# Optimization experiments

Hardware: AMD Instinct MI355X
Metric: run time of the kernel (lower is better)

## Reference

```python
import jax, jax.numpy as jnp
import numpy as np

N = 50000   # num nodes
E = 800000  # num edges
D_IN, D_HID, D_OUT = 128, 128, 64


def setup_inputs() -> dict:
    key = jax.random.key(0)
    ks = jax.random.split(key, 10)
    x = jax.random.normal(ks[0], (N, D_IN), dtype=jnp.float32)
    edge_index = jax.random.randint(ks[1], (2, E), 0, N, dtype=jnp.int32)
    edge_weight = jax.random.uniform(ks[2], (E,), dtype=jnp.float32)
    def lin(k, fan_in, fan_out):
        bound = 1.0 / np.sqrt(fan_in)
        kw, kb = jax.random.split(k)
        W = jax.random.uniform(kw, (fan_out, fan_in), minval=-bound, maxval=bound, dtype=jnp.float32)
        b = jax.random.uniform(kb, (fan_out,), minval=-bound, maxval=bound, dtype=jnp.float32)
        return W, b
    W0, b0 = lin(ks[3], 2 * D_IN, D_HID)
    W1, b1 = lin(ks[4], 2 * D_HID, D_HID)
    W2, b2 = lin(ks[5], 2 * D_HID, D_OUT)
    return {"x": x, "edge_index": edge_index, "edge_weight": edge_weight,
            "W0": W0, "b0": b0, "W1": W1, "b1": b1, "W2": W2, "b2": b2}


def _sage_layer(x, row, col, ew, W, b):
    # weighted mean aggregation over incoming edges (dst = row, src = col)
    n = x.shape[0]
    msg = x[col] * ew[:, None]                      # [E, D] gather + scale
    agg = jax.ops.segment_sum(msg, row, num_segments=n)    # [N, D]
    deg = jax.ops.segment_sum(ew, row, num_segments=n)     # [N]
    deg = jnp.clip(deg, 1.0, None)[:, None]
    h = jnp.concatenate([x, agg / deg], axis=-1)    # [N, 2D]
    return h @ W.T + b


def reference(x, edge_index, edge_weight, W0, b0, W1, b1, W2, b2):
    row, col = edge_index[0], edge_index[1]
    h = jax.nn.relu(_sage_layer(x, row, col, edge_weight, W0, b0))
    h = jax.nn.relu(_sage_layer(h, row, col, edge_weight, W1, b1))
    return _sage_layer(h, row, col, edge_weight, W2, b2)
```

## Files before the change

### kernel.cpp

```cpp
#include <hip/hip_runtime.h>


#define D 128
#define K2 256
#define NQ 4
#define QW 12500
#define NBUCK 196
#define SCAP 5120
#define CH 2048

typedef __attribute__((ext_vector_type(8))) short short8;
typedef __attribute__((ext_vector_type(4))) float floatx4;

__device__ inline unsigned short rne_bf16(float f) {
    unsigned int u = __float_as_uint(f);
    u += 0x7fffu + ((u >> 16) & 1u);
    return (unsigned short)(u >> 16);
}

__device__ inline int quarter_of(int c) {
    return (c >= 2 * QW) ? ((c >= 3 * QW) ? 3 : 2) : ((c >= QW) ? 1 : 0);
}

__global__ void prep_kernel(const float* __restrict__ x, unsigned short* __restrict__ x_hi,
                            const float* __restrict__ W0, const float* __restrict__ W1,
                            const float* __restrict__ W2,
                            unsigned short* __restrict__ h0, unsigned short* __restrict__ l0,
                            unsigned short* __restrict__ h1, unsigned short* __restrict__ l1,
                            unsigned short* __restrict__ h2, unsigned short* __restrict__ l2,
                            const int* __restrict__ row, const int* __restrict__ col,
                            int* __restrict__ cnt, int n4, int E) {
    int b = blockIdx.x;
    int tid = threadIdx.x;
    if (b < 6250) {
        int i = b * 256 + tid;
        if (i < n4) {
            float4 v = reinterpret_cast<const float4*>(x)[i];
            ushort4 o;
            o.x = rne_bf16(v.x); o.y = rne_bf16(v.y); o.z = rne_bf16(v.z); o.w = rne_bf16(v.w);
            reinterpret_cast<ushort4*>(x_hi)[i] = o;
        }
    } else if (b < 6570) {
        int i = (b - 6250) * 256 + tid;
        const float* w; unsigned short *hi, *lo; int sidx, didx;
        if (i < 32768)      { w = W0; hi = h0; lo = l0; sidx = i; didx = i; }
        else if (i < 65536) { w = W1; hi = h1; lo = l1; sidx = i - 32768; didx = sidx; }
        else if (i < 81920) {
            w = W2; hi = h2; lo = l2;
            int i2 = i - 65536;
            int r = i2 >> 7, k = i2 & 127;
            sidx = (r < 64) ? (r * 256 + k) : ((r - 64) * 256 + 128 + k);
            didx = i2;
        }
        else return;
        float f = w[sidx];
        unsigned short h = rne_bf16(f);
        float fh = __uint_as_float(((unsigned int)h) << 16);
        hi[didx] = h;
        lo[didx] = rne_bf16(f - fh);
    } else {
        int e = (b - 6570) * 256 + tid;
        if (e < E) {
            int key = row[e] * NQ + quarter_of(col[e]);
            atomicAdd(&cnt[key], 1);
        }
    }
}

__global__ void scan1_kernel(const int* __restrict__ cnt, int* __restrict__ rowptr,
                             int* __restrict__ bsum, int NB) {
    __shared__ int s[256];
    int tid = threadIdx.x;
    int gid = blockIdx.x * 256 + tid;
    int v = (gid < NB) ? cnt[gid] : 0;
    s[tid] = v;
    __syncthreads();
    for (int off = 1; off < 256; off <<= 1) {
        int t = (tid >= off) ? s[tid - off] : 0;
        __syncthreads();
        s[tid] += t;
        __syncthreads();
    }
    if (gid < NB) rowptr[gid] = s[tid] - v;
    if (tid == 255) bsum[blockIdx.x] = s[255];
}

__global__ void scan2_kernel(int* __restrict__ bsum, int* __restrict__ boff, int nb) {
    __shared__ int s[1024];
    int tid = threadIdx.x;
    int v = (tid < nb) ? bsum[tid] : 0;
    s[tid] = v;
    __syncthreads();
    for (int off = 1; off < 1024; off <<= 1) {
        int t = (tid >= off) ? s[tid - off] : 0;
        __syncthreads();
        s[tid] += t;
        __syncthreads();
    }
    if (tid < nb) boff[tid] = s[tid] - v;
}

__global__ void scan3_kernel(int* __restrict__ rowptr, const int* __restrict__ boff,
                             int* __restrict__ cursor, int NB, int E) {
    int gid = blockIdx.x * 256 + threadIdx.x;
    if (gid < NB) {
        int v = rowptr[gid] + boff[gid >> 8];
        rowptr[gid] = v;
        cursor[gid] = v;
    } else if (gid == NB) {
        rowptr[NB] = E;
    }
}

__global__ __launch_bounds__(512) void scatter_bin(
    const int* __restrict__ row, const int* __restrict__ col,
    const float* __restrict__ ew, int* __restrict__ scnt,
    int* __restrict__ cursor, int2* __restrict__ stage,
    int2* __restrict__ ep, int E) {
    __shared__ int cnt[NBUCK];
    __shared__ int base[NBUCK];
    __shared__ int gb[NBUCK];
    __shared__ int scn[256];
    __shared__ int2 sdata[CH];
    __shared__ unsigned char sbkt[CH];
    int tid = threadIdx.x;
    for (int i = tid; i < NBUCK; i += 512) cnt[i] = 0;
    __syncthreads();

    int e0 = blockIdx.x * CH + tid * 4;
    int rw4[4], c4[4], w4[4], b4[4], lo4[4];
    bool act = (e0 < E);
    if (act) {
        int4 r = *reinterpret_cast<const int4*>(row + e0);
        int4 c = *reinterpret_cast<const int4*>(col + e0);
        float4 w = *reinterpret_cast<const float4*>(ew + e0);
        rw4[0] = r.x; rw4[1] = r.y; rw4[2] = r.z; rw4[3] = r.w;
        c4[0] = c.x; c4[1] = c.y; c4[2] = c.z; c4[3] = c.w;
        w4[0] = __float_as_int(w.x); w4[1] = __float_as_int(w.y);
        w4[2] = __float_as_int(w.z); w4[3] = __float_as_int(w.w);
#pragma unroll
        for (int u = 0; u < 4; u++) {
            b4[u] = rw4[u] >> 8;
            lo4[u] = atomicAdd(&cnt[b4[u]], 1);
        }
    }
    __syncthreads();

    if (tid < 256) scn[tid] = (tid < NBUCK) ? cnt[tid] : 0;
    __syncthreads();
    for (int off = 1; off < 256; off <<= 1) {
        int t = (tid >= off && tid < 256) ? scn[tid - off] : 0;
        __syncthreads();
        if (tid < 256) scn[tid] += t;
        __syncthreads();
    }
    if (tid < NBUCK) {
        base[tid] = scn[tid] - cnt[tid];
        gb[tid] = (cnt[tid] > 0) ? atomicAdd(&scnt[tid], cnt[tid]) : 0;
    }
    __syncthreads();

    if (act) {
#pragma unroll
        for (int u = 0; u < 4; u++) {
            int slot = base[b4[u]] + lo4[u];
            int key = ((rw4[u] & 255) << 2) | quarter_of(c4[u]);
            sdata[slot] = make_int2((key << 16) | c4[u], w4[u]);
            sbkt[slot] = (unsigned char)b4[u];
        }
    }
    __syncthreads();

    int total = scn[255];
    for (int i = tid; i < total; i += 512) {
        int b = sbkt[i];
        int2 rec = sdata[i];
        int pos = gb[b] + (i - base[b]);
        if (pos < SCAP) {
            stage[b * SCAP + pos] = rec;
        } else {
            int binidx = (b << 10) + ((unsigned int)rec.x >> 16);
            int p = atomicAdd(&cursor[binidx], 1);
            ep[p] = make_int2(rec.x & 0xFFFF, rec.y);
        }
    }
}

__global__ __launch_bounds__(512) void scatter_drain(
    const int2* __restrict__ stage, const int* __restrict__ scnt,
    const int* __restrict__ cursor, int2* __restrict__ ep, int NBtot) {
    __shared__ int cur[1024];
    int b = blockIdx.x;
    int tid = threadIdx.x;
    for (int i = tid; i < 1024; i += 512) {
        int g = (b << 10) + i;
        cur[i] = (g < NBtot) ? cursor[g] : 0;
    }
    __syncthreads();
    int m = scnt[b];
    if (m > SCAP) m = SCAP;
    for (int i = tid; i < m; i += 512) {
        int2 rec = stage[b * SCAP + i];
        int key = (unsigned int)rec.x >> 16;
        int p = atomicAdd(&cur[key], 1);
        ep[p] = make_int2(rec.x & 0xFFFF, rec.y);
    }
}

__device__ inline void accum8(float* acc, uint4 a, float w) {
    acc[0] += __uint_as_float(a.x << 16) * w;
    acc[1] += __uint_as_float(a.x & 0xffff0000u) * w;
    acc[2] += __uint_as_float(a.y << 16) * w;
    acc[3] += __uint_as_float(a.y & 0xffff0000u) * w;
    acc[4] += __uint_as_float(a.z << 16) * w;
    acc[5] += __uint_as_float(a.z & 0xffff0000u) * w;
    acc[6] += __uint_as_float(a.w << 16) * w;
    acc[7] += __uint_as_float(a.w & 0xffff0000u) * w;
}

__global__ void gather_agg_bf(const unsigned short* __restrict__ src, const int* __restrict__ rowptr4,
                              const int2* __restrict__ ep, unsigned short* __restrict__ agg, int N) {
    long long t = (long long)blockIdx.x * blockDim.x + threadIdx.x;
    int wid = (int)(t >> 6);
    int lane = threadIdx.x & 63;
    int slot = lane >> 4;
    int fl = lane & 15;
    int n = wid * 4 + slot;
    if (n >= N) return;
    int beg = rowptr4[n * 4], end = rowptr4[n * 4 + 4];
    float acc[8];
#pragma unroll
    for (int j = 0; j < 8; j++) acc[j] = 0.f;
    float ds = 0.f;
    int e = beg;
    for (; e + 7 < end; e += 8) {
        int2 p[8];
#pragma unroll
        for (int u = 0; u < 8; u++) p[u] = ep[e + u];
        uint4 a[8];
#pragma unroll
        for (int u = 0; u < 8; u++)
            a[u] = *reinterpret_cast<const uint4*>(src + (size_t)p[u].x * D + fl * 8);
#pragma unroll
        for (int u = 0; u < 8; u++) {
            float w = __int_as_float(p[u].y);
            accum8(acc, a[u], w);
            ds += w;
        }
    }
    for (; e + 3 < end; e += 4) {
        int2 p[4];
#pragma unroll
        for (int u = 0; u < 4; u++) p[u] = ep[e + u];
#pragma unroll
        for (int u = 0; u < 4; u++) {
            uint4 a = *reinterpret_cast<const uint4*>(src + (size_t)p[u].x * D + fl * 8);
            float w = __int_as_float(p[u].y);
            accum8(acc, a, w);
            ds += w;
        }
    }
    for (; e < end; ++e) {
        int2 p = ep[e];
        uint4 a = *reinterpret_cast<const uint4*>(src + (size_t)p.x * D + fl * 8);
        float w = __int_as_float(p.y);
        accum8(acc, a, w);
        ds += w;
    }
    float inv = 1.0f / (ds > 1.f ? ds : 1.f);
    uint4 o;
    o.x = (unsigned int)rne_bf16(acc[0] * inv) | ((unsigned int)rne_bf16(acc[1] * inv) << 16);
    o.y = (unsigned int)rne_bf16(acc[2] * inv) | ((unsigned int)rne_bf16(acc[3] * inv) << 16);
    o.z = (unsigned int)rne_bf16(acc[4] * inv) | ((unsigned int)rne_bf16(acc[5] * inv) << 16);
    o.w = (unsigned int)rne_bf16(acc[6] * inv) | ((unsigned int)rne_bf16(acc[7] * inv) << 16);
    *reinterpret_cast<uint4*>(agg + (size_t)n * D + fl * 8) = o;
}

template<bool RELU, bool BF16OUT, int OSTRIDE>
__global__ __launch_bounds__(256) void sage_gemm(
    const unsigned short* __restrict__ src, const unsigned short* __restrict__ agg,
    const unsigned short* __restrict__ Whi, const unsigned short* __restrict__ Wlo,
    const float* __restrict__ bias, float* __restrict__ outf,
    unsigned short* __restrict__ outb, int N) {
    __shared__ short sW[2][32][260];
    int tid = threadIdx.x;
    int c0 = blockIdx.y * 32;

    for (int i = tid; i < 2048; i += 256) {
        int h = i >> 10;
        int rem = i & 1023;
        int r = rem & 31;
        int k8 = rem >> 5;
        const unsigned short* wp = (h ? Wlo : Whi) + (size_t)(c0 + r) * K2 + k8 * 8;
        *reinterpret_cast<uint4*>(&sW[h][r][k8 * 8]) = *reinterpret_cast<const uint4*>(wp);
    }
    __syncthreads();

    int lane = tid & 63;
    int wv = tid >> 6;
    int nlane = lane & 15;
    int quad = lane >> 4;
    int m0 = blockIdx.x * 128 + wv * 32;
    int r0 = m0 + nlane;      if (r0 >= N) r0 = N - 1;
    int r1 = m0 + 16 + nlane; if (r1 >= N) r1 = N - 1;

    short8 a[2][8];
#pragma unroll
    for (int ks = 0; ks < 8; ks++) {
        int k0 = ks * 32;
        const unsigned short* p0 = (k0 < D) ? (src + (size_t)r0 * D + k0)
                                            : (agg + (size_t)r0 * D + (k0 - D));
        const unsigned short* p1 = (k0 < D) ? (src + (size_t)r1 * D + k0)
                                            : (agg + (size_t)r1 * D + (k0 - D));
        a[0][ks] = *reinterpret_cast<const short8*>(p0 + quad * 8);
        a[1][ks] = *reinterpret_cast<const short8*>(p1 + quad * 8);
    }

    floatx4 acc[2][2];
#pragma unroll
    for (int mt = 0; mt < 2; mt++)
#pragma unroll
        for (int nt = 0; nt < 2; nt++) acc[mt][nt] = (floatx4){0.f, 0.f, 0.f, 0.f};

#pragma unroll
    for (int ks = 0; ks < 8; ks++) {
        int k0 = ks * 32;
#pragma unroll
        for (int nt = 0; nt < 2; nt++) {
            short8 bh = *reinterpret_cast<const short8*>(&sW[0][nt * 16 + nlane][k0 + quad * 8]);
            short8 bl = *reinterpret_cast<const short8*>(&sW[1][nt * 16 + nlane][k0 + quad * 8]);
            acc[0][nt] = __builtin_amdgcn_mfma_f32_16x16x32_bf16(a[0][ks], bh, acc[0][nt], 0, 0, 0);
            acc[0][nt] = __builtin_amdgcn_mfma_f32_16x16x32_bf16(a[0][ks], bl, acc[0][nt], 0, 0, 0);
            acc[1][nt] = __builtin_amdgcn_mfma_f32_16x16x32_bf16(a[1][ks], bh, acc[1][nt], 0, 0, 0);
            acc[1][nt] = __builtin_amdgcn_mfma_f32_16x16x32_bf16(a[1][ks], bl, acc[1][nt], 0, 0, 0);
        }
    }

#pragma unroll
    for (int nt = 0; nt < 2; nt++) {
        int c = c0 + nt * 16 + nlane;
        float bb = bias[c];
#pragma unroll
        for (int mt = 0; mt < 2; mt++) {
#pragma unroll
            for (int r = 0; r < 4; r++) {
                int node = m0 + mt * 16 + quad * 4 + r;
                if (node < N) {
                    float y = acc[mt][nt][r] + bb;
                    if (RELU) y = y > 0.f ? y : 0.f;
                    if (BF16OUT) outb[(size_t)node * OSTRIDE + c] = rne_bf16(y);
                    else         outf[(size_t)node * OSTRIDE + c] = y;
                }
            }
        }
    }
}

__global__ __launch_bounds__(256) void sage_gemm2(
    const unsigned short* __restrict__ h1, const unsigned short* __restrict__ Whi,
    const unsigned short* __restrict__ Wlo, const float* __restrict__ b2,
    float* __restrict__ ytop2, unsigned short* __restrict__ z2, int N) {
    __shared__ short sW[2][32][132];
    int tid = threadIdx.x;
    int c0 = blockIdx.y * 32;

    for (int i = tid; i < 1024; i += 256) {
        int h = i >> 9;
        int rem = i & 511;
        int r = rem & 31;
        int k8 = rem >> 5;
        const unsigned short* wp = (h ? Wlo : Whi) + (size_t)(c0 + r) * 128 + k8 * 8;
        *reinterpret_cast<uint4*>(&sW[h][r][k8 * 8]) = *reinterpret_cast<const uint4*>(wp);
    }
    __syncthreads();

    int lane = tid & 63;
    int wv = tid >> 6;
    int nlane = lane & 15;
    int quad = lane >> 4;
    int m0 = blockIdx.x * 128 + wv * 32;
    int r0 = m0 + nlane;      if (r0 >= N) r0 = N - 1;
    int r1 = m0 + 16 + nlane; if (r1 >= N) r1 = N - 1;

    short8 a[2][4];
#pragma unroll
    for (int ks = 0; ks < 4; ks++) {
        a[0][ks] = *reinterpret_cast<const short8*>(h1 + (size_t)r0 * D + ks * 32 + quad * 8);
        a[1][ks] = *reinterpret_cast<const short8*>(h1 + (size_t)r1 * D + ks * 32 + quad * 8);
    }

    floatx4 acc[2][2];
#pragma unroll
    for (int mt = 0; mt < 2; mt++)
#pragma unroll
        for (int nt = 0; nt < 2; nt++) acc[mt][nt] = (floatx4){0.f, 0.f, 0.f, 0.f};

#pragma unroll
    for (int ks = 0; ks < 4; ks++) {
        int k0 = ks * 32;
#pragma unroll
        for (int nt = 0; nt < 2; nt++) {
            short8 bh = *reinterpret_cast<const short8*>(&sW[0][nt * 16 + nlane][k0 + quad * 8]);
            short8 bl = *reinterpret_cast<const short8*>(&sW[1][nt * 16 + nlane][k0 + quad * 8]);
            acc[0][nt] = __builtin_amdgcn_mfma_f32_16x16x32_bf16(a[0][ks], bh, acc[0][nt], 0, 0, 0);
            acc[0][nt] = __builtin_amdgcn_mfma_f32_16x16x32_bf16(a[0][ks], bl, acc[0][nt], 0, 0, 0);
            acc[1][nt] = __builtin_amdgcn_mfma_f32_16x16x32_bf16(a[1][ks], bh, acc[1][nt], 0, 0, 0);
            acc[1][nt] = __builtin_amdgcn_mfma_f32_16x16x32_bf16(a[1][ks], bl, acc[1][nt], 0, 0, 0);
        }
    }

#pragma unroll
    for (int nt = 0; nt < 2; nt++) {
        int c = c0 + nt * 16 + nlane;
#pragma unroll
        for (int mt = 0; mt < 2; mt++) {
#pragma unroll
            for (int r = 0; r < 4; r++) {
                int node = m0 + mt * 16 + quad * 4 + r;
                if (node < N) {
                    float v = acc[mt][nt][r];
                    if (c < 64) ytop2[(size_t)node * 64 + c] = v + b2[c];
                    else        z2[(size_t)node * 64 + (c - 64)] = rne_bf16(v);
                }
            }
        }
    }
}

__global__ void gather_out(const unsigned short* __restrict__ z2, const int* __restrict__ rowptr4,
                           const int2* __restrict__ ep, const float* __restrict__ ytop2,
                           float* __restrict__ out, int N) {
    long long t = (long long)blockIdx.x * blockDim.x + threadIdx.x;
    int wid = (int)(t >> 6);
    int lane = threadIdx.x & 63;
    int slot = lane >> 3;
    int fl = lane & 7;
    int n = wid * 8 + slot;
    if (n >= N) return;
    int beg = rowptr4[n * 4], end = rowptr4[n * 4 + 4];
    float acc[8];
#pragma unroll
    for (int j = 0; j < 8; j++) acc[j] = 0.f;
    float ds = 0.f;
    int e = beg;
    for (; e + 7 < end; e += 8) {
        int2 p[8];
#pragma unroll
        for (int u = 0; u < 8; u++) p[u] = ep[e + u];
        uint4 a[8];
#pragma unroll
        for (int u = 0; u < 8; u++)
            a[u] = *reinterpret_cast<const uint4*>(z2 + (size_t)p[u].x * 64 + fl * 8);
#pragma unroll
        for (int u = 0; u < 8; u++) {
            float w = __int_as_float(p[u].y);
            accum8(acc, a[u], w);
            ds += w;
        }
    }
    for (; e < end; ++e) {
        int2 p = ep[e];
        uint4 a = *reinterpret_cast<const uint4*>(z2 + (size_t)p.x * 64 + fl * 8);
        float w = __int_as_float(p.y);
        accum8(acc, a, w);
        ds += w;
    }
    float inv = 1.0f / (ds > 1.f ? ds : 1.f);
    const float* yt = ytop2 + (size_t)n * 64 + fl * 8;
    float* op = out + (size_t)n * 64 + fl * 8;
    float4 t0 = *reinterpret_cast<const float4*>(yt);
    float4 t1 = *reinterpret_cast<const float4*>(yt + 4);
    float4 o0 = make_float4(t0.x + acc[0] * inv, t0.y + acc[1] * inv,
                            t0.z + acc[2] * inv, t0.w + acc[3] * inv);
    float4 o1 = make_float4(t1.x + acc[4] * inv, t1.y + acc[5] * inv,
                            t1.z + acc[6] * inv, t1.w + acc[7] * inv);
    *reinterpret_cast<float4*>(op) = o0;
    *reinterpret_cast<float4*>(op + 4) = o1;
}

extern "C" void kernel_launch(void* const* d_in, const int* in_sizes, int n_in,
                              void* d_out, int out_size, void* d_ws, size_t ws_size,
                              hipStream_t stream) {
    const float* x  = (const float*)d_in[0];
    const int*   ei = (const int*)d_in[1];
    const float* ew = (const float*)d_in[2];
    const float* W0 = (const float*)d_in[3];
    const float* b0 = (const float*)d_in[4];
    const float* W1 = (const float*)d_in[5];
    const float* b1 = (const float*)d_in[6];
    const float* W2 = (const float*)d_in[7];
    const float* b2 = (const float*)d_in[8];
    float* out = (float*)d_out;

    const int N = 50000;
    const int E = in_sizes[2];
    const int NB = N * NQ;
    const int* row = ei;
    const int* col = ei + E;

    char* base = (char*)d_ws;
    size_t ND = (size_t)N * D;
    unsigned short* x_hi   = (unsigned short*)base;               base += ND * 2;
    unsigned short* h0_hi  = (unsigned short*)base;               base += ND * 2;
    unsigned short* h1_hi  = (unsigned short*)base;               base += ND * 2;
    unsigned short* agg_hi = (unsigned short*)base;               base += ND * 2;
    int2* ep               = (int2*)base;                         base += (size_t)E * 8;
    int* rowptr4           = (int*)base;                          base += (size_t)(NB + 1) * 4;
    unsigned short* W0hi   = (unsigned short*)base;               base += 128 * 256 * 2;
    unsigned short* W0lo   = (unsigned short*)base;               base += 128 * 256 * 2;
    unsigned short* W1hi   = (unsigned short*)base;               base += 128 * 256 * 2;
    unsigned short* W1lo   = (unsigned short*)base;               base += 128 * 256 * 2;
    unsigned short* W2Chi  = (unsigned short*)base;               base += 128 * 128 * 2;
    unsigned short* W2Clo  = (unsigned short*)base;               base += 128 * 128 * 2;

    int* cnt    = (int*)h0_hi;
    int* cursor = cnt + NB;
    int* bsum   = cursor + NB;
    int* boff   = bsum + 1024;
    int* scnt   = boff + 1024;

    int2* stage = (int2*)h1_hi;

    float* ytop2          = (float*)agg_hi;
    unsigned short* z2    = (unsigned short*)h0_hi;

    int nbScan = (NB + 255) / 256;

    hipMemsetAsync(cnt, 0, (size_t)(2 * NB + 2304) * sizeof(int), stream);
    int n4 = (int)(ND / 4);
    prep_kernel<<<9695, 256, 0, stream>>>(x, x_hi, W0, W1, W2,
        W0hi, W0lo, W1hi, W1lo, W2Chi, W2Clo, row, col, cnt, n4, E);

    scan1_kernel<<<nbScan, 256, 0, stream>>>(cnt, rowptr4, bsum, NB);
    scan2_kernel<<<1, 1024, 0, stream>>>(bsum, boff, nbScan);
    scan3_kernel<<<(NB + 256) / 256 + 1, 256, 0, stream>>>(rowptr4, boff, cursor, NB, E);
    scatter_bin<<<(E + CH - 1) / CH, 512, 0, stream>>>(row, col, ew, scnt, cursor, stage, ep, E);
    scatter_drain<<<NBUCK, 512, 0, stream>>>(stage, scnt, cursor, ep, NB);

    int nWaves = (N + 3) / 4;
    int aggBlocks = (int)(((long long)nWaves * 64 + 255) / 256);
    int nodeTiles = (N + 127) / 128;
    dim3 g128(nodeTiles, 4);

    gather_agg_bf<<<aggBlocks, 256, 0, stream>>>(x_hi, rowptr4, ep, agg_hi, N);
    sage_gemm<true, true, D><<<g128, 256, 0, stream>>>(
        x_hi, agg_hi, W0hi, W0lo, b0, nullptr, h0_hi, N);

    gather_agg_bf<<<aggBlocks, 256, 0, stream>>>(h0_hi, rowptr4, ep, agg_hi, N);
    sage_gemm<true, true, D><<<g128, 256, 0, stream>>>(
        h0_hi, agg_hi, W1hi, W1lo, b1, nullptr, h1_hi, N);

    sage_gemm2<<<g128, 256, 0, stream>>>(h1_hi, W2Chi, W2Clo, b2, ytop2, z2, N);
    int nWaves2 = (N + 7) / 8;
    int outBlocks = (int)(((long long)nWaves2 * 64 + 255) / 256);
    gather_out<<<outBlocks, 256, 0, stream>>>(z2, rowptr4, ep, ytop2, out, N);
}
```

Baseline: 307.2 us.

## Fuse neighbor aggregation and SAGE GEMM into one per-tile layer kernel

Replaces the separate gather-aggregate kernel and the GEMM kernel for layers 0 and 1 with one kernel per 128-node tile. Each tile aggregates neighbor rows into shared memory and then runs the MFMA GEMM over all four 32-column output tiles, reloading weights each pass. This removes the global round trip of the aggregate buffer and two launches per layer. In exchange the grid is much smaller (about 391 blocks of 512 threads), weights are streamed serially per block, and gather latency can no longer overlap with GEMM work from other launches.

```diff
diff --git a/kernel.cpp b/kernel.cpp
--- a/kernel.cpp
+++ b/kernel.cpp
@@ -218,141 +218,135 @@
     acc[7] += __uint_as_float(a.w & 0xffff0000u) * w;
 }
 
-__global__ void gather_agg_bf(const unsigned short* __restrict__ src, const int* __restrict__ rowptr4,
-                              const int2* __restrict__ ep, unsigned short* __restrict__ agg, int N) {
-    long long t = (long long)blockIdx.x * blockDim.x + threadIdx.x;
-    int wid = (int)(t >> 6);
-    int lane = threadIdx.x & 63;
-    int slot = lane >> 4;
-    int fl = lane & 15;
-    int n = wid * 4 + slot;
-    if (n >= N) return;
-    int beg = rowptr4[n * 4], end = rowptr4[n * 4 + 4];
-    float acc[8];
-#pragma unroll
-    for (int j = 0; j < 8; j++) acc[j] = 0.f;
-    float ds = 0.f;
-    int e = beg;
-    for (; e + 7 < end; e += 8) {
-        int2 p[8];
-#pragma unroll
-        for (int u = 0; u < 8; u++) p[u] = ep[e + u];
-        uint4 a[8];
-#pragma unroll
-        for (int u = 0; u < 8; u++)
-            a[u] = *reinterpret_cast<const uint4*>(src + (size_t)p[u].x * D + fl * 8);
-#pragma unroll
-        for (int u = 0; u < 8; u++) {
-            float w = __int_as_float(p[u].y);
-            accum8(acc, a[u], w);
-            ds += w;
-        }
-    }
-    for (; e + 3 < end; e += 4) {
-        int2 p[4];
-#pragma unroll
-        for (int u = 0; u < 4; u++) p[u] = ep[e + u];
-#pragma unroll
-        for (int u = 0; u < 4; u++) {
-            uint4 a = *reinterpret_cast<const uint4*>(src + (size_t)p[u].x * D + fl * 8);
-            float w = __int_as_float(p[u].y);
-            accum8(acc, a, w);
-            ds += w;
-        }
-    }
-    for (; e < end; ++e) {
-        int2 p = ep[e];
-        uint4 a = *reinterpret_cast<const uint4*>(src + (size_t)p.x * D + fl * 8);
-        float w = __int_as_float(p.y);
-        accum8(acc, a, w);
-        ds += w;
-    }
-    float inv = 1.0f / (ds > 1.f ? ds : 1.f);
-    uint4 o;
-    o.x = (unsigned int)rne_bf16(acc[0] * inv) | ((unsigned int)rne_bf16(acc[1] * inv) << 16);
-    o.y = (unsigned int)rne_bf16(acc[2] * inv) | ((unsigned int)rne_bf16(acc[3] * inv) << 16);
-    o.z = (unsigned int)rne_bf16(acc[4] * inv) | ((unsigned int)rne_bf16(acc[5] * inv) << 16);
-    o.w = (unsigned int)rne_bf16(acc[6] * inv) | ((unsigned int)rne_bf16(acc[7] * inv) << 16);
-    *reinterpret_cast<uint4*>(agg + (size_t)n * D + fl * 8) = o;
-}
-
-template<bool RELU, bool BF16OUT, int OSTRIDE>
-__global__ __launch_bounds__(256) void sage_gemm(
-    const unsigned short* __restrict__ src, const unsigned short* __restrict__ agg,
-    const unsigned short* __restrict__ Whi, const unsigned short* __restrict__ Wlo,
-    const float* __restrict__ bias, float* __restrict__ outf,
+__global__ __launch_bounds__(512) void fused_layer(
+    const unsigned short* __restrict__ src, const int* __restrict__ rowptr4,
+    const int2* __restrict__ ep, const unsigned short* __restrict__ Whi,
+    const unsigned short* __restrict__ Wlo, const float* __restrict__ bias,
     unsigned short* __restrict__ outb, int N) {
-    __shared__ short sW[2][32][260];
-    int tid = threadIdx.x;
-    int c0 = blockIdx.y * 32;
-
-    for (int i = tid; i < 2048; i += 256) {
-        int h = i >> 10;
-        int rem = i & 1023;
-        int r = rem & 31;
-        int k8 = rem >> 5;
-        const unsigned short* wp = (h ? Wlo : Whi) + (size_t)(c0 + r) * K2 + k8 * 8;
-        *reinterpret_cast<uint4*>(&sW[h][r][k8 * 8]) = *reinterpret_cast<const uint4*>(wp);
-    }
-    __syncthreads();
-
+    __shared__ char smem[128 * 136 * 2];
+    short (*aggL)[136] = reinterpret_cast<short (*)[136]>(smem);
+    short (*sW)[32][260] = reinterpret_cast<short (*)[32][260]>(smem);
+
+    int tid = threadIdx.x;
     int lane = tid & 63;
     int wv = tid >> 6;
     int nlane = lane & 15;
     int quad = lane >> 4;
-    int m0 = blockIdx.x * 128 + wv * 32;
-    int r0 = m0 + nlane;      if (r0 >= N) r0 = N - 1;
-    int r1 = m0 + 16 + nlane; if (r1 >= N) r1 = N - 1;
-
-    short8 a[2][8];
-#pragma unroll
-    for (int ks = 0; ks < 8; ks++) {
-        int k0 = ks * 32;
-        const unsigned short* p0 = (k0 < D) ? (src + (size_t)r0 * D + k0)
-                                            : (agg + (size_t)r0 * D + (k0 - D));
-        const unsigned short* p1 = (k0 < D) ? (src + (size_t)r1 * D + k0)
-                                            : (agg + (size_t)r1 * D + (k0 - D));
-        a[0][ks] = *reinterpret_cast<const short8*>(p0 + quad * 8);
-        a[1][ks] = *reinterpret_cast<const short8*>(p1 + quad * 8);
-    }
-
-    floatx4 acc[2][2];
-#pragma unroll
-    for (int mt = 0; mt < 2; mt++)
-#pragma unroll
-        for (int nt = 0; nt < 2; nt++) acc[mt][nt] = (floatx4){0.f, 0.f, 0.f, 0.f};
-
-#pragma unroll
-    for (int ks = 0; ks < 8; ks++) {
-        int k0 = ks * 32;
+    int m0 = blockIdx.x * 128;
+
+    int rs = m0 + wv * 16 + nlane; if (rs >= N) rs = N - 1;
+    short8 a[8];
+#pragma unroll
+    for (int ks = 0; ks < 4; ks++)
+        a[ks] = *reinterpret_cast<const short8*>(src + (size_t)rs * D + ks * 32 + quad * 8);
+
+    int slot = lane >> 4;
+    int fl = lane & 15;
+#pragma unroll
+    for (int g = 0; g < 4; g++) {
+        int n_local = g * 32 + wv * 4 + slot;
+        int n = m0 + n_local;
+        int beg = 0, end = 0;
+        if (n < N) { beg = rowptr4[n * 4]; end = rowptr4[n * 4 + 4]; }
+        float acc[8];
+#pragma unroll
+        for (int j = 0; j < 8; j++) acc[j] = 0.f;
+        float ds = 0.f;
+        int e = beg;
+        for (; e + 7 < end; e += 8) {
+            int2 p[8];
+#pragma unroll
+            for (int u = 0; u < 8; u++) p[u] = ep[e + u];
+            uint4 av[8];
+#pragma unroll
+            for (int u = 0; u < 8; u++)
+                av[u] = *reinterpret_cast<const uint4*>(src + (size_t)p[u].x * D + fl * 8);
+#pragma unroll
+            for (int u = 0; u < 8; u++) {
+                float w = __int_as_float(p[u].y);
+                accum8(acc, av[u], w);
+                ds += w;
+            }
+        }
+        for (; e + 3 < end; e += 4) {
+            int2 p[4];
+#pragma unroll
+            for (int u = 0; u < 4; u++) p[u] = ep[e + u];
+#pragma unroll
+            for (int u = 0; u < 4; u++) {
+                uint4 av = *reinterpret_cast<const uint4*>(src + (size_t)p[u].x * D + fl * 8);
+                float w = __int_as_float(p[u].y);
+                accum8(acc, av, w);
+                ds += w;
+            }
+        }
+        for (; e < end; ++e) {
+            int2 p = ep[e];
+            uint4 av = *reinterpret_cast<const uint4*>(src + (size_t)p.x * D + fl * 8);
+            float w = __int_as_float(p.y);
+            accum8(acc, av, w);
+            ds += w;
+        }
+        float inv = 1.0f / (ds > 1.f ? ds : 1.f);
+        uint4 o;
+        o.x = (unsigned int)rne_bf16(acc[0] * inv) | ((unsigned int)rne_bf16(acc[1] * inv) << 16);
+        o.y = (unsigned int)rne_bf16(acc[2] * inv) | ((unsigned int)rne_bf16(acc[3] * inv) << 16);
+        o.z = (unsigned int)rne_bf16(acc[4] * inv) | ((unsigned int)rne_bf16(acc[5] * inv) << 16);
+        o.w = (unsigned int)rne_bf16(acc[6] * inv) | ((unsigned int)rne_bf16(acc[7] * inv) << 16);
+        *reinterpret_cast<uint4*>(&aggL[n_local][fl * 8]) = o;
+    }
+    __syncthreads();
+
+    int rl = wv * 16 + nlane;
+#pragma unroll
+    for (int ks = 4; ks < 8; ks++)
+        a[ks] = *reinterpret_cast<const short8*>(&aggL[rl][(ks - 4) * 32 + quad * 8]);
+    __syncthreads();
+
+    int node_base = m0 + wv * 16 + quad * 4;
+#pragma unroll 1
+    for (int ct = 0; ct < 4; ct++) {
+        int c0 = ct * 32;
+        for (int i = tid; i < 2048; i += 512) {
+            int h = i >> 10;
+            int rem = i & 1023;
+            int r = rem & 31;
+            int k8 = rem >> 5;
+            const unsigned short* wp = (h ? Wlo : Whi) + (size_t)(c0 + r) * K2 + k8 * 8;
+            *reinterpret_cast<uint4*>(&sW[h][r][k8 * 8]) = *reinterpret_cast<const uint4*>(wp);
+        }
+        __syncthreads();
+
+        floatx4 acc[2];
+#pragma unroll
+        for (int nt = 0; nt < 2; nt++) acc[nt] = (floatx4){0.f, 0.f, 0.f, 0.f};
+#pragma unroll
+        for (int ks = 0; ks < 8; ks++) {
+            int k0 = ks * 32;
+#pragma unroll
+            for (int nt = 0; nt < 2; nt++) {
+                short8 bh = *reinterpret_cast<const short8*>(&sW[0][nt * 16 + nlane][k0 + quad * 8]);
+                short8 bl = *reinterpret_cast<const short8*>(&sW[1][nt * 16 + nlane][k0 + quad * 8]);
+                acc[nt] = __builtin_amdgcn_mfma_f32_16x16x32_bf16(a[ks], bh, acc[nt], 0, 0, 0);
+                acc[nt] = __builtin_amdgcn_mfma_f32_16x16x32_bf16(a[ks], bl, acc[nt], 0, 0, 0);
+            }
+        }
+
 #pragma unroll
         for (int nt = 0; nt < 2; nt++) {
-            short8 bh = *reinterpret_cast<const short8*>(&sW[0][nt * 16 + nlane][k0 + quad * 8]);
-            short8 bl = *reinterpret_cast<const short8*>(&sW[1][nt * 16 + nlane][k0 + quad * 8]);
-            acc[0][nt] = __builtin_amdgcn_mfma_f32_16x16x32_bf16(a[0][ks], bh, acc[0][nt], 0, 0, 0);
-            acc[0][nt] = __builtin_amdgcn_mfma_f32_16x16x32_bf16(a[0][ks], bl, acc[0][nt], 0, 0, 0);
-            acc[1][nt] = __builtin_amdgcn_mfma_f32_16x16x32_bf16(a[1][ks], bh, acc[1][nt], 0, 0, 0);
-            acc[1][nt] = __builtin_amdgcn_mfma_f32_16x16x32_bf16(a[1][ks], bl, acc[1][nt], 0, 0, 0);
-        }
-    }
-
-#pragma unroll
-    for (int nt = 0; nt < 2; nt++) {
-        int c = c0 + nt * 16 + nlane;
-        float bb = bias[c];
-#pragma unroll
-        for (int mt = 0; mt < 2; mt++) {
+            int c = c0 + nt * 16 + nlane;
+            float bb = bias[c];
 #pragma unroll
             for (int r = 0; r < 4; r++) {
-                int node = m0 + mt * 16 + quad * 4 + r;
+                int node = node_base + r;
                 if (node < N) {
-                    float y = acc[mt][nt][r] + bb;
-                    if (RELU) y = y > 0.f ? y : 0.f;
-                    if (BF16OUT) outb[(size_t)node * OSTRIDE + c] = rne_bf16(y);
-                    else         outf[(size_t)node * OSTRIDE + c] = y;
+                    float y = acc[nt][r] + bb;
+                    y = y > 0.f ? y : 0.f;
+                    outb[(size_t)node * D + c] = rne_bf16(y);
                 }
             }
         }
+        __syncthreads();
     }
 }
 
@@ -537,19 +531,13 @@
     scatter_bin<<<(E + CH - 1) / CH, 512, 0, stream>>>(row, col, ew, scnt, cursor, stage, ep, E);
     scatter_drain<<<NBUCK, 512, 0, stream>>>(stage, scnt, cursor, ep, NB);
 
-    int nWaves = (N + 3) / 4;
-    int aggBlocks = (int)(((long long)nWaves * 64 + 255) / 256);
     int nodeTiles = (N + 127) / 128;
+
+    fused_layer<<<nodeTiles, 512, 0, stream>>>(x_hi, rowptr4, ep, W0hi, W0lo, b0, h0_hi, N);
+
+    fused_layer<<<nodeTiles, 512, 0, stream>>>(h0_hi, rowptr4, ep, W1hi, W1lo, b1, h1_hi, N);
+
     dim3 g128(nodeTiles, 4);
-
-    gather_agg_bf<<<aggBlocks, 256, 0, stream>>>(x_hi, rowptr4, ep, agg_hi, N);
-    sage_gemm<true, true, D><<<g128, 256, 0, stream>>>(
-        x_hi, agg_hi, W0hi, W0lo, b0, nullptr, h0_hi, N);
-
-    gather_agg_bf<<<aggBlocks, 256, 0, stream>>>(h0_hi, rowptr4, ep, agg_hi, N);
-    sage_gemm<true, true, D><<<g128, 256, 0, stream>>>(
-        h0_hi, agg_hi, W1hi, W1lo, b1, nullptr, h1_hi, N);
-
     sage_gemm2<<<g128, 256, 0, stream>>>(h1_hi, W2Chi, W2Clo, b2, ytop2, z2, N);
     int nWaves2 = (N + 7) / 8;
     int outBlocks = (int)(((long long)nWaves2 * 64 + 255) / 256);
```

After: 430.8 us. 1.4x slower.

## Build CSR row pointers inside drain via per-bucket histograms, dropping global count and scans

Applied to the files above, without the earlier changes.

Removes the global per-(row,quarter) atomic count pass in prep and the three-kernel global prefix scan. Row offsets are now computed after binning: one small kernel scans the per-bucket counts, and each drain block builds a local 1024-entry histogram and scan to write rowptr and place edges. Stage overflow now goes to a bounded overflow list that every drain block scans, instead of using global cursors. The overflow list is capped at OCAP entries, so overflow beyond that capacity would silently drop edges, and every drain block rereads the whole overflow list.

```diff
diff --git a/kernel.cpp b/kernel.cpp
--- a/kernel.cpp
+++ b/kernel.cpp
@@ -7,6 +7,7 @@
 #define QW 12500
 #define NBUCK 196
 #define SCAP 5120
+#define OCAP 8192
 #define CH 2048
 
 typedef __attribute__((ext_vector_type(8))) short short8;
@@ -28,8 +29,7 @@
                             unsigned short* __restrict__ h0, unsigned short* __restrict__ l0,
                             unsigned short* __restrict__ h1, unsigned short* __restrict__ l1,
                             unsigned short* __restrict__ h2, unsigned short* __restrict__ l2,
-                            const int* __restrict__ row, const int* __restrict__ col,
-                            int* __restrict__ cnt, int n4, int E) {
+                            int n4) {
     int b = blockIdx.x;
     int tid = threadIdx.x;
     if (b < 6250) {
@@ -40,7 +40,7 @@
             o.x = rne_bf16(v.x); o.y = rne_bf16(v.y); o.z = rne_bf16(v.z); o.w = rne_bf16(v.w);
             reinterpret_cast<ushort4*>(x_hi)[i] = o;
         }
-    } else if (b < 6570) {
+    } else {
         int i = (b - 6250) * 256 + tid;
         const float* w; unsigned short *hi, *lo; int sidx, didx;
         if (i < 32768)      { w = W0; hi = h0; lo = l0; sidx = i; didx = i; }
@@ -58,65 +58,14 @@
         float fh = __uint_as_float(((unsigned int)h) << 16);
         hi[didx] = h;
         lo[didx] = rne_bf16(f - fh);
-    } else {
-        int e = (b - 6570) * 256 + tid;
-        if (e < E) {
-            int key = row[e] * NQ + quarter_of(col[e]);
-            atomicAdd(&cnt[key], 1);
-        }
-    }
-}
-
-__global__ void scan1_kernel(const int* __restrict__ cnt, int* __restrict__ rowptr,
-                             int* __restrict__ bsum, int NB) {
-    __shared__ int s[256];
-    int tid = threadIdx.x;
-    int gid = blockIdx.x * 256 + tid;
-    int v = (gid < NB) ? cnt[gid] : 0;
-    s[tid] = v;
-    __syncthreads();
-    for (int off = 1; off < 256; off <<= 1) {
-        int t = (tid >= off) ? s[tid - off] : 0;
-        __syncthreads();
-        s[tid] += t;
-        __syncthreads();
-    }
-    if (gid < NB) rowptr[gid] = s[tid] - v;
-    if (tid == 255) bsum[blockIdx.x] = s[255];
-}
-
-__global__ void scan2_kernel(int* __restrict__ bsum, int* __restrict__ boff, int nb) {
-    __shared__ int s[1024];
-    int tid = threadIdx.x;
-    int v = (tid < nb) ? bsum[tid] : 0;
-    s[tid] = v;
-    __syncthreads();
-    for (int off = 1; off < 1024; off <<= 1) {
-        int t = (tid >= off) ? s[tid - off] : 0;
-        __syncthreads();
-        s[tid] += t;
-        __syncthreads();
-    }
-    if (tid < nb) boff[tid] = s[tid] - v;
-}
-
-__global__ void scan3_kernel(int* __restrict__ rowptr, const int* __restrict__ boff,
-                             int* __restrict__ cursor, int NB, int E) {
-    int gid = blockIdx.x * 256 + threadIdx.x;
-    if (gid < NB) {
-        int v = rowptr[gid] + boff[gid >> 8];
-        rowptr[gid] = v;
-        cursor[gid] = v;
-    } else if (gid == NB) {
-        rowptr[NB] = E;
     }
 }
 
 __global__ __launch_bounds__(512) void scatter_bin(
     const int* __restrict__ row, const int* __restrict__ col,
     const float* __restrict__ ew, int* __restrict__ scnt,
-    int* __restrict__ cursor, int2* __restrict__ stage,
-    int2* __restrict__ ep, int E) {
+    int* __restrict__ novf, int4* __restrict__ ovf,
+    int2* __restrict__ stage, int E) {
     __shared__ int cnt[NBUCK];
     __shared__ int base[NBUCK];
     __shared__ int gb[NBUCK];
@@ -179,31 +128,87 @@
         if (pos < SCAP) {
             stage[b * SCAP + pos] = rec;
         } else {
-            int binidx = (b << 10) + ((unsigned int)rec.x >> 16);
-            int p = atomicAdd(&cursor[binidx], 1);
-            ep[p] = make_int2(rec.x & 0xFFFF, rec.y);
-        }
-    }
+            int idx = atomicAdd(novf, 1);
+            if (idx < OCAP)
+                ovf[idx] = make_int4((b << 10) | ((unsigned int)rec.x >> 16),
+                                     rec.x & 0xFFFF, rec.y, 0);
+        }
+    }
+}
+
+__global__ void bucket_scan(const int* __restrict__ scnt, int* __restrict__ bucketBase,
+                            int* __restrict__ rowptr, int NB, int E) {
+    __shared__ int s[256];
+    int tid = threadIdx.x;
+    int v = (tid < NBUCK) ? scnt[tid] : 0;
+    s[tid] = v;
+    __syncthreads();
+    for (int off = 1; off < 256; off <<= 1) {
+        int t = (tid >= off) ? s[tid - off] : 0;
+        __syncthreads();
+        s[tid] += t;
+        __syncthreads();
+    }
+    if (tid < NBUCK) bucketBase[tid] = s[tid] - v;
+    if (tid == 0) rowptr[NB] = E;
 }
 
 __global__ __launch_bounds__(512) void scatter_drain(
     const int2* __restrict__ stage, const int* __restrict__ scnt,
-    const int* __restrict__ cursor, int2* __restrict__ ep, int NBtot) {
-    __shared__ int cur[1024];
+    const int* __restrict__ bucketBase, const int* __restrict__ novf_p,
+    const int4* __restrict__ ovf, int* __restrict__ rowptr,
+    int2* __restrict__ ep, int NB) {
+    __shared__ int hist[1024];
+    __shared__ int s[512];
     int b = blockIdx.x;
     int tid = threadIdx.x;
-    for (int i = tid; i < 1024; i += 512) {
-        int g = (b << 10) + i;
-        cur[i] = (g < NBtot) ? cursor[g] : 0;
-    }
-    __syncthreads();
-    int m = scnt[b];
-    if (m > SCAP) m = SCAP;
+    for (int i = tid; i < 1024; i += 512) hist[i] = 0;
+    __syncthreads();
+
+    int m = scnt[b]; if (m > SCAP) m = SCAP;
+    for (int i = tid; i < m; i += 512) {
+        int2 rec = stage[b * SCAP + i];
+        atomicAdd(&hist[(unsigned int)rec.x >> 16], 1);
+    }
+    int nov = *novf_p; if (nov > OCAP) nov = OCAP;
+    for (int i = tid; i < nov; i += 512) {
+        int4 r = ovf[i];
+        if ((r.x >> 10) == b) atomicAdd(&hist[r.x & 1023], 1);
+    }
+    __syncthreads();
+
+    int a0 = hist[2 * tid], a1 = hist[2 * tid + 1];
+    s[tid] = a0 + a1;
+    __syncthreads();
+    for (int off = 1; off < 512; off <<= 1) {
+        int t = (tid >= off) ? s[tid - off] : 0;
+        __syncthreads();
+        s[tid] += t;
+        __syncthreads();
+    }
+    int P = s[tid] - (a0 + a1);
+    int base = bucketBase[b];
+    int e0 = base + P;
+    int e1 = e0 + a0;
+    hist[2 * tid] = e0;
+    hist[2 * tid + 1] = e1;
+    int g0 = (b << 10) + 2 * tid;
+    if (g0 < NB)     rowptr[g0] = e0;
+    if (g0 + 1 < NB) rowptr[g0 + 1] = e1;
+    __syncthreads();
+
     for (int i = tid; i < m; i += 512) {
         int2 rec = stage[b * SCAP + i];
         int key = (unsigned int)rec.x >> 16;
-        int p = atomicAdd(&cur[key], 1);
+        int p = atomicAdd(&hist[key], 1);
         ep[p] = make_int2(rec.x & 0xFFFF, rec.y);
+    }
+    for (int i = tid; i < nov; i += 512) {
+        int4 r = ovf[i];
+        if ((r.x >> 10) == b) {
+            int p = atomicAdd(&hist[r.x & 1023], 1);
+            ep[p] = make_int2(r.y, r.z);
+        }
     }
 }
 
@@ -513,29 +518,24 @@
     unsigned short* W2Chi  = (unsigned short*)base;               base += 128 * 128 * 2;
     unsigned short* W2Clo  = (unsigned short*)base;               base += 128 * 128 * 2;
 
-    int* cnt    = (int*)h0_hi;
-    int* cursor = cnt + NB;
-    int* bsum   = cursor + NB;
-    int* boff   = bsum + 1024;
-    int* scnt   = boff + 1024;
+    int* scnt       = (int*)h0_hi;
+    int* novf       = scnt + 256;
+    int* bucketBase = scnt + 320;
+    int4* ovf       = (int4*)(scnt + 1024);
 
     int2* stage = (int2*)h1_hi;
 
     float* ytop2          = (float*)agg_hi;
     unsigned short* z2    = (unsigned short*)h0_hi;
 
-    int nbScan = (NB + 255) / 256;
-
-    hipMemsetAsync(cnt, 0, (size_t)(2 * NB + 2304) * sizeof(int), stream);
+    hipMemsetAsync(scnt, 0, 2048, stream);
     int n4 = (int)(ND / 4);
-    prep_kernel<<<9695, 256, 0, stream>>>(x, x_hi, W0, W1, W2,
-        W0hi, W0lo, W1hi, W1lo, W2Chi, W2Clo, row, col, cnt, n4, E);
-
-    scan1_kernel<<<nbScan, 256, 0, stream>>>(cnt, rowptr4, bsum, NB);
-    scan2_kernel<<<1, 1024, 0, stream>>>(bsum, boff, nbScan);
-    scan3_kernel<<<(NB + 256) / 256 + 1, 256, 0, stream>>>(rowptr4, boff, cursor, NB, E);
-    scatter_bin<<<(E + CH - 1) / CH, 512, 0, stream>>>(row, col, ew, scnt, cursor, stage, ep, E);
-    scatter_drain<<<NBUCK, 512, 0, stream>>>(stage, scnt, cursor, ep, NB);
+    prep_kernel<<<6570, 256, 0, stream>>>(x, x_hi, W0, W1, W2,
+        W0hi, W0lo, W1hi, W1lo, W2Chi, W2Clo, n4);
+
+    scatter_bin<<<(E + CH - 1) / CH, 512, 0, stream>>>(row, col, ew, scnt, novf, ovf, stage, E);
+    bucket_scan<<<1, 256, 0, stream>>>(scnt, bucketBase, rowptr4, NB, E);
+    scatter_drain<<<NBUCK, 512, 0, stream>>>(stage, scnt, bucketBase, novf, ovf, rowptr4, ep, NB);
 
     int nWaves = (N + 3) / 4;
     int aggBlocks = (int)(((long long)nWaves * 64 + 255) / 256);
```

Result: faster. 273.0 us (-11.1%).
